# Kernel optimization log

Hardware: AMD Instinct MI355X
Metric: run time of the kernel (lower is better)

Reference implementation:

```python
import jax, jax.numpy as jnp
import numpy as np

BODY_EDGES = [(0, 2), (0, 5), (2, 7), (5, 8), (11, 12), (0, 11), (0, 12), (7, 11), (8, 12), (11, 13), (13, 15), (12, 14), (14, 16), (11, 23), (12, 24), (23, 24), (11, 24), (12, 23)]
N_JOINTS = 33
N_FEAT = 52
HIDDEN = 128
BN_EPS = 1e-5


def _make_adj():
    a = np.eye(N_JOINTS, dtype=np.float32)
    for i, j in BODY_EDGES:
        a[i, j] = 1.0
        a[j, i] = 1.0
    deg = np.clip(a.sum(1), 1.0, None)
    d = deg ** -0.5
    return jnp.asarray(d[:, None] * a * d[None, :])


def setup_inputs() -> dict:
    key = jax.random.key(0)
    ks = iter(jax.random.split(key, 40))
    B, T = 64, 256
    def lin(k, i, o):
        return jax.random.normal(k, (i, o), jnp.float32) / np.sqrt(i)
    inp = {
        'x': jax.random.normal(next(ks), (B, T, N_JOINTS, N_FEAT), jnp.float32),
        'adj': _make_adj(),
        # layer 0: in 52 -> out 128 (has skip linear)
        'W0': lin(next(ks), N_FEAT, HIDDEN), 'b0': jax.random.normal(next(ks), (HIDDEN,)) * 0.02,
        'S0': lin(next(ks), N_FEAT, HIDDEN), 'sb0': jax.random.normal(next(ks), (HIDDEN,)) * 0.02,
        'g0': 1.0 + 0.1 * jax.random.normal(next(ks), (HIDDEN,)), 'be0': 0.1 * jax.random.normal(next(ks), (HIDDEN,)),
        'm0': 0.1 * jax.random.normal(next(ks), (HIDDEN,)), 'v0': 1.0 + 0.1 * jax.random.uniform(next(ks), (HIDDEN,)),
        # layers 1,2: 128 -> 128 (identity skip)
        'W1': lin(next(ks), HIDDEN, HIDDEN), 'b1': jax.random.normal(next(ks), (HIDDEN,)) * 0.02,
        'g1': 1.0 + 0.1 * jax.random.normal(next(ks), (HIDDEN,)), 'be1': 0.1 * jax.random.normal(next(ks), (HIDDEN,)),
        'm1': 0.1 * jax.random.normal(next(ks), (HIDDEN,)), 'v1': 1.0 + 0.1 * jax.random.uniform(next(ks), (HIDDEN,)),
        'W2': lin(next(ks), HIDDEN, HIDDEN), 'b2': jax.random.normal(next(ks), (HIDDEN,)) * 0.02,
        'g2': 1.0 + 0.1 * jax.random.normal(next(ks), (HIDDEN,)), 'be2': 0.1 * jax.random.normal(next(ks), (HIDDEN,)),
        'm2': 0.1 * jax.random.normal(next(ks), (HIDDEN,)), 'v2': 1.0 + 0.1 * jax.random.uniform(next(ks), (HIDDEN,)),
        # temporal attention MLP: 128 -> 128 -> 1
        'tW1': lin(next(ks), HIDDEN, HIDDEN), 'tb1': jax.random.normal(next(ks), (HIDDEN,)) * 0.02,
        'tW2': lin(next(ks), HIDDEN, 1), 'tb2': jax.random.normal(next(ks), (1,)) * 0.02,
    }
    return inp


def _gcn(h, adj, W, b, g, be, m, v, skip):
    # adjacency mix: [B*T, J, D_in]
    a = jnp.einsum('nm,bmd->bnd', adj, h)
    z = a @ W + b
    z = (z - m) * jax.lax.rsqrt(v + BN_EPS) * g + be  # eval-mode BatchNorm1d
    return jax.nn.gelu(z, approximate=False) + skip


def reference(x, adj, W0, b0, S0, sb0, g0, be0, m0, v0,
              W1, b1, g1, be1, m1, v1,
              W2, b2, g2, be2, m2, v2,
              tW1, tb1, tW2, tb2):
    B, T, J, Fd = x.shape
    h = x.reshape(B * T, J, Fd)
    h = _gcn(h, adj, W0, b0, g0, be0, m0, v0, h @ S0 + sb0)
    h = _gcn(h, adj, W1, b1, g1, be1, m1, v1, h)
    h = _gcn(h, adj, W2, b2, g2, be2, m2, v2, h)
    # dropout inactive (eval mode)
    xt = h.mean(axis=1).reshape(B, T, -1)                  # [B, T, H]
    score = jax.nn.gelu(xt @ tW1 + tb1, approximate=False) @ tW2 + tb2  # [B, T, 1]
    attn = jax.nn.softmax(score, axis=1)
    return (xt * attn).sum(axis=1)                         # [B, H]
```

## Files before the change

### kernel.cpp

```cpp
#include <hip/hip_runtime.h>
#include <hip/hip_bf16.h>
#include <math.h>


#define NJ 33
#define NF 52
#define NH 128
#define NT 256
#define NB 64
#define NSAMP (NB*NT)
#define SPB 2
#define NBLKS (NSAMP/SPB)
#define HSTR 136
#define PSTR 40

typedef unsigned short u16;
typedef _Float16 f16;
typedef f16   half8 __attribute__((ext_vector_type(8)));
typedef f16   h2    __attribute__((ext_vector_type(2)));
typedef float f32x4 __attribute__((ext_vector_type(4)));

#define HO_W0    0
#define HO_S0    8192
#define HO_W1    16384
#define HO_W2    32768
#define HO_TW1   49152
#define HO_ADJ32 65536
#define H_TOTAL  66560
#define FO_BASE  (H_TOTAL/2)
#define FO_A0    (FO_BASE+0)
#define FO_SB0   (FO_BASE+768)
#define FO_TB1   (FO_BASE+896)
#define FO_TW2   (FO_BASE+1024)
#define FO_XT    (FO_BASE+1152)
#define FO_SC    (FO_XT + NSAMP*NH)

__device__ __forceinline__ float bf2f(u16 u) { return __uint_as_float(((unsigned)u) << 16); }
__device__ __forceinline__ float ldv(const void* p, long i, int f) {
    float r;
    if (f) r = bf2f(((const u16*)p)[i]);
    else   r = ((const float*)p)[i];
    return r;
}
__device__ int detect_bf16(const void* p) {
    const u16* q = (const u16*)p;
    int nz = 0, ok = 0;
#pragma unroll
    for (int k = 0; k < 64; k++) {
        u16 u = q[k];
        if (u & 0x7FFF) {
            nz++;
            int e = (u >> 7) & 0xFF;
            ok += (e >= 0x40 && e <= 0xBF) ? 1 : 0;
        }
    }
    return (nz == 0) || (ok * 20 >= nz * 19);
}

__device__ __forceinline__ float gelu_t(float x) {
    float xc = fminf(fmaxf(x, -8.f), 8.f);
    float u  = xc * fmaf(xc * xc, 0.10294324f, 2.3022082f);
#if __has_builtin(__builtin_amdgcn_exp2f)
    float e  = __builtin_amdgcn_exp2f(u);
#else
    float e  = exp2f(u);
#endif
#if __has_builtin(__builtin_amdgcn_rcpf)
    float tt = (e - 1.f) * __builtin_amdgcn_rcpf(e + 1.f);
#else
    float tt = (e - 1.f) / (e + 1.f);
#endif
    float hx = 0.5f * x;
    return fmaf(hx, tt, hx);
}

#define MFMA16(a, b, c) __builtin_amdgcn_mfma_f32_16x16x32_f16(a, b, c, 0, 0, 0)

__global__ __launch_bounds__(256) void prep(
    const void* adj,
    const void* W0, const void* b0, const void* S0, const void* sb0,
    const void* g0, const void* be0, const void* m0, const void* v0,
    const void* W1, const void* b1, const void* g1, const void* be1, const void* m1, const void* v1,
    const void* W2, const void* b2, const void* g2, const void* be2, const void* m2, const void* v2,
    const void* tW1, const void* tb1, const void* tW2,
    void* ws)
{
    f16* H = (f16*)ws; float* F = (float*)ws;
    const int bi = blockIdx.x, t = threadIdx.x;
    if (bi == 0) {
        const int fW = detect_bf16(W0), fS = detect_bf16(S0);
        for (int i = t; i < NF * 128; i += 256) {
            int k = i >> 7, n = i & 127;
            H[HO_W0 + n * 64 + k] = (f16)ldv(W0, i, fW);
            H[HO_S0 + n * 64 + k] = (f16)ldv(S0, i, fS);
        }
        for (int i = t; i < 128 * 16; i += 256) {
            int n = i >> 4, k = 48 + (i & 15);
            if (k >= NF) { H[HO_W0 + n * 64 + k] = (f16)0.f; H[HO_S0 + n * 64 + k] = (f16)0.f; }
        }
    } else if (bi == 1) {
        const int f = detect_bf16(W1);
        for (int i = t; i < 128 * 128; i += 256) {
            int k = i >> 7, n = i & 127;
            H[HO_W1 + n * 128 + k] = (f16)ldv(W1, i, f);
        }
    } else if (bi == 2) {
        const int f = detect_bf16(W2);
        for (int i = t; i < 128 * 128; i += 256) {
            int k = i >> 7, n = i & 127;
            H[HO_W2 + n * 128 + k] = (f16)ldv(W2, i, f);
        }
    } else if (bi == 3) {
        const int f = detect_bf16(tW1);
        for (int i = t; i < 128 * 128; i += 256) {
            int k = i >> 7, n = i & 127;
            H[HO_TW1 + n * 128 + k] = (f16)ldv(tW1, i, f);
        }
    } else {
        if (t < 128) {
            int c = t;
            {
                float g = ldv(g0,c,detect_bf16(g0)), be = ldv(be0,c,detect_bf16(be0));
                float m = ldv(m0,c,detect_bf16(m0)), v = ldv(v0,c,detect_bf16(v0));
                float b = ldv(b0,c,detect_bf16(b0));
                float A = g * rsqrtf(v + 1e-5f);
                F[FO_A0 + 0*256 + c] = A; F[FO_A0 + 0*256 + 128 + c] = (b - m)*A + be;
            }
            {
                float g = ldv(g1,c,detect_bf16(g1)), be = ldv(be1,c,detect_bf16(be1));
                float m = ldv(m1,c,detect_bf16(m1)), v = ldv(v1,c,detect_bf16(v1));
                float b = ldv(b1,c,detect_bf16(b1));
                float A = g * rsqrtf(v + 1e-5f);
                F[FO_A0 + 1*256 + c] = A; F[FO_A0 + 1*256 + 128 + c] = (b - m)*A + be;
            }
            {
                float g = ldv(g2,c,detect_bf16(g2)), be = ldv(be2,c,detect_bf16(be2));
                float m = ldv(m2,c,detect_bf16(m2)), v = ldv(v2,c,detect_bf16(v2));
                float b = ldv(b2,c,detect_bf16(b2));
                float A = g * rsqrtf(v + 1e-5f);
                F[FO_A0 + 2*256 + c] = A; F[FO_A0 + 2*256 + 128 + c] = (b - m)*A + be;
            }
            F[FO_SB0 + c] = ldv(sb0, c, detect_bf16(sb0));
            F[FO_TB1 + c] = ldv(tb1, c, detect_bf16(tb1));
            F[FO_TW2 + c] = ldv(tW2, c, detect_bf16(tW2));
        }
        const int fA = detect_bf16(adj);
        for (int i = t; i < 1024; i += 256) {
            int r = i >> 5, c = i & 31;
            float v = (r < 25 && c < 25) ? ldv(adj, (long)r*NJ + c, fA) : 0.f;
            H[HO_ADJ32 + i] = (f16)v;
        }
    }
}

#define PTWRITE(ACC)                                                            \
    _Pragma("unroll")                                                           \
    for (int mt = 0; mt < 4; mt++) {                                            \
        const int fF = mt >> 1;                                                 \
        const int jb = (mt & 1) * 16;                                           \
        _Pragma("unroll")                                                       \
        for (int nt = 0; nt < 2; nt++) {                                        \
            f16* pp = Pt + (fF*128 + (nt ? c1 : c0))*PSTR;                      \
            _Pragma("unroll")                                                   \
            for (int r2 = 0; r2 < 4; r2 += 2) {                                 \
                int j0 = jb + q*4 + r2;                                         \
                if (j0 + 1 < 25) {                                              \
                    h2 v2w = { (f16)ACC[mt][nt][r2], (f16)ACC[mt][nt][r2+1] };  \
                    *(h2*)(pp + j0) = v2w;                                      \
                } else if (j0 < 25) {                                           \
                    pp[j0] = (f16)ACC[mt][nt][r2];                              \
                }                                                               \
            }                                                                   \
        }                                                                       \
    }

#define ADJEPI(L, WRHB) {                                                       \
    f32x4 zac[2][2][2];                                                         \
    _Pragma("unroll")                                                           \
    for (int fF = 0; fF < 2; fF++) {                                            \
        _Pragma("unroll")                                                       \
        for (int nt = 0; nt < 2; nt++) {                                        \
            half8 bz = *(const half8*)(Pt + (fF*128 + (nt?c1:c0))*PSTR + q*8);  \
            zac[fF][0][nt] = MFMA16(afadj0, bz, z4);                            \
            zac[fF][1][nt] = MFMA16(afadj1, bz, z4);                            \
        }                                                                       \
    }                                                                           \
    _Pragma("unroll")                                                           \
    for (int nt = 0; nt < 2; nt++) {                                            \
        const int cc = nt ? c1 : c0;                                            \
        const float Av = rA[L][nt], Dv = rD[L][nt];                             \
        _Pragma("unroll")                                                       \
        for (int fF = 0; fF < 2; fF++) {                                        \
            _Pragma("unroll")                                                   \
            for (int m2 = 0; m2 < 2; m2++) {                                    \
                _Pragma("unroll")                                               \
                for (int r4 = 0; r4 < 4; r4++) {                                \
                    float zv = (m2 == 0) ? zac[fF][0][nt][r4]                   \
                             : (jlt[r4] ? zac[fF][1][nt][r4]                    \
                                        : acc[2*fF+1][nt][r4]);                 \
                    float hnew = gelu_t(fmaf(zv, Av, Dv)) + hz[fF][m2][nt][r4]; \
                    hz[fF][m2][nt][r4] = hnew;                                  \
                    if (WRHB)                                                   \
                        hb[((2*fF+m2)*16 + q*4 + r4)*HSTR + cc] = (f16)hnew;    \
                }                                                               \
            }                                                                   \
            {                                                                   \
                float hnew = gelu_t(fmaf(acc[4][nt][fF], Av, Dv)) + h32[fF][nt];\
                h32[fF][nt] = (q == 0) ? hnew : 0.f;                            \
                if (WRHB && q == 0)                                             \
                    hb[(64 + fF)*HSTR + cc] = (f16)hnew;                        \
            }                                                                   \
        }                                                                       \
    }                                                                           \
}

#define GEMM128(WOFF)                                                           \
    {                                                                           \
        half8 bf[2][4];                                                         \
        _Pragma("unroll")                                                       \
        for (int nt = 0; nt < 2; nt++)                                          \
            _Pragma("unroll")                                                   \
            for (int ks = 0; ks < 4; ks++)                                      \
                bf[nt][ks] = *(const half8*)(HW + (WOFF) + (nt?c1:c0)*128 + ks*32 + q*8); \
        _Pragma("unroll")                                                       \
        for (int mt = 0; mt < 5; mt++) { acc[mt][0] = z4; acc[mt][1] = z4; }    \
        _Pragma("unroll")                                                       \
        for (int mt = 0; mt < 5; mt++) {                                        \
            const int m = mt*16 + ml;                                           \
            _Pragma("unroll")                                                   \
            for (int ks = 0; ks < 4; ks++) {                                    \
                half8 af = *(const half8*)(hb + m*HSTR + ks*32 + q*8);          \
                acc[mt][0] = MFMA16(af, bf[0][ks], acc[mt][0]);                 \
                acc[mt][1] = MFMA16(af, bf[1][ks], acc[mt][1]);                 \
            }                                                                   \
        }                                                                       \
    }

__global__ __launch_bounds__(256) void gcn_mfma(const void* __restrict__ x,
                                                void* __restrict__ ws)
{
    const f16* HW = (const f16*)ws;
    float* F = (float*)ws;
    float* xt_g = F + FO_XT;
    float* sc_g = F + FO_SC;

    __shared__ __align__(16) f16 hb[80 * HSTR];
    __shared__ __align__(16) f16 Pt[2 * 128 * PSTR];
    __shared__ float rbuf4[4];
    __shared__ int sfx;
    float* xtb = (float*)Pt;

    const int t = threadIdx.x, lane = t & 63, wv = t >> 6;
    const int q = lane >> 4, ml = lane & 15;
    const int n0 = wv * 32;
    const int c0 = n0 + ml, c1 = n0 + 16 + ml;
    const f32x4 z4 = {0.f, 0.f, 0.f, 0.f};
    const bool jlt[4] = { q <= 2, q <= 1, q <= 1, q <= 1 };
    const half8 zero8 = {(f16)0.f,(f16)0.f,(f16)0.f,(f16)0.f,(f16)0.f,(f16)0.f,(f16)0.f,(f16)0.f};

    if (t == 0) sfx = detect_bf16(x);
#pragma unroll
    for (int i = t; i < 512; i += 256) {
        int fF = i >> 8, rem = i & 255, n = rem >> 1, ch = rem & 1;
        *(half8*)(Pt + (fF*128 + n)*PSTR + 24 + ch*8) = zero8;
    }

    float rA[3][2], rD[3][2];
#pragma unroll
    for (int L = 0; L < 3; L++) {
        rA[L][0] = F[FO_A0 + L*256 + c0];        rA[L][1] = F[FO_A0 + L*256 + c1];
        rD[L][0] = F[FO_A0 + L*256 + 128 + c0];  rD[L][1] = F[FO_A0 + L*256 + 128 + c1];
    }
    const float sb0a = F[FO_SB0 + c0], sb0b = F[FO_SB0 + c1];
    half8 afadj0 = *(const half8*)(HW + HO_ADJ32 + ml*32 + q*8);
    half8 afadj1 = *(const half8*)(HW + HO_ADJ32 + (16+ml)*32 + q*8);
    __syncthreads();

    {
        const int fX = sfx;
        const long xb = (long)blockIdx.x * (SPB * NJ * NF);
#pragma unroll 1
        for (int it = 0; it < 3; it++) {
            int g = t + it * 256;
            if (g < 66 * 8) {
                int r = g >> 3, blk = g & 7;
                int fF = (r >= 33) ? 1 : 0;
                int j = r - 33 * fF;
                int fr = (j < 32) ? (fF * 32 + j) : (64 + fF);
                half8 o;
                if (!fX) {
                    const float* base = (const float*)x + xb + (long)r * NF + blk * 8;
                    if (blk < 6) {
                        float4 v0 = *(const float4*)base;
                        float4 v1 = *(const float4*)(base + 4);
                        o[0]=(f16)v0.x; o[1]=(f16)v0.y; o[2]=(f16)v0.z; o[3]=(f16)v0.w;
                        o[4]=(f16)v1.x; o[5]=(f16)v1.y; o[6]=(f16)v1.z; o[7]=(f16)v1.w;
                    } else if (blk == 6) {
                        float4 v0 = *(const float4*)base;
                        o = zero8;
                        o[0]=(f16)v0.x; o[1]=(f16)v0.y; o[2]=(f16)v0.z; o[3]=(f16)v0.w;
                    } else o = zero8;
                } else {
                    long rb = xb + (long)r * NF;
#pragma unroll
                    for (int i = 0; i < 8; i++) {
                        int cx = blk * 8 + i;
                        o[i] = (f16)(cx < NF ? bf2f(((const u16*)x)[rb + cx]) : 0.f);
                    }
                }
                *(half8*)(hb + fr * HSTR + blk * 8) = o;
            }
        }
    }
    __syncthreads();

    f32x4 acc[5][2];
    float hz[2][2][2][4];
    float h32[2][2];

    {
        half8 bw[2][2], bs[2][2];
#pragma unroll
        for (int nt = 0; nt < 2; nt++) {
            int n = nt ? c1 : c0;
#pragma unroll
            for (int ks = 0; ks < 2; ks++) {
                bw[nt][ks] = *(const half8*)(HW + HO_W0 + n*64 + ks*32 + q*8);
                bs[nt][ks] = *(const half8*)(HW + HO_S0 + n*64 + ks*32 + q*8);
            }
        }
        f32x4 acs[5][2];
#pragma unroll
        for (int mt = 0; mt < 5; mt++) { acc[mt][0]=z4; acc[mt][1]=z4; acs[mt][0]=z4; acs[mt][1]=z4; }
#pragma unroll
        for (int mt = 0; mt < 5; mt++) {
            const int m = mt*16 + ml;
            half8 a0 = *(const half8*)(hb + m*HSTR + q*8);
            half8 a1 = *(const half8*)(hb + m*HSTR + 32 + q*8);
            acc[mt][0] = MFMA16(a0, bw[0][0], acc[mt][0]);
            acc[mt][0] = MFMA16(a1, bw[0][1], acc[mt][0]);
            acc[mt][1] = MFMA16(a0, bw[1][0], acc[mt][1]);
            acc[mt][1] = MFMA16(a1, bw[1][1], acc[mt][1]);
            acs[mt][0] = MFMA16(a0, bs[0][0], acs[mt][0]);
            acs[mt][0] = MFMA16(a1, bs[0][1], acs[mt][0]);
            acs[mt][1] = MFMA16(a0, bs[1][0], acs[mt][1]);
            acs[mt][1] = MFMA16(a1, bs[1][1], acs[mt][1]);
        }
        __syncthreads();
        PTWRITE(acc)
#pragma unroll
        for (int fF = 0; fF < 2; fF++)
#pragma unroll
            for (int m2 = 0; m2 < 2; m2++)
#pragma unroll
                for (int nt = 0; nt < 2; nt++)
#pragma unroll
                    for (int r4 = 0; r4 < 4; r4++)
                        hz[fF][m2][nt][r4] = acs[2*fF+m2][nt][r4] + (nt ? sb0b : sb0a);
#pragma unroll
        for (int fF = 0; fF < 2; fF++)
#pragma unroll
            for (int nt = 0; nt < 2; nt++)
                h32[fF][nt] = (q == 0) ? (acs[4][nt][fF] + (nt ? sb0b : sb0a)) : 0.f;
        ADJEPI(0, 1)
        __syncthreads();
    }

    GEMM128(HO_W1)
    __syncthreads();
    PTWRITE(acc)
    ADJEPI(1, 1)
    __syncthreads();

    GEMM128(HO_W2)
    __syncthreads();
    PTWRITE(acc)
    ADJEPI(2, 0)
    __syncthreads();

#pragma unroll
    for (int fF = 0; fF < 2; fF++)
#pragma unroll
        for (int nt = 0; nt < 2; nt++) {
            float s = h32[fF][nt];
#pragma unroll
            for (int m2 = 0; m2 < 2; m2++)
#pragma unroll
                for (int r4 = 0; r4 < 4; r4++) s += hz[fF][m2][nt][r4];
            s += __shfl_xor(s, 16, 64);
            s += __shfl_xor(s, 32, 64);
            float xtc = s * (1.0f / 33.0f);
            if (q == 0) {
                int cc = nt ? c1 : c0;
                xtb[fF * 128 + cc] = xtc;
                xt_g[((long)blockIdx.x * SPB + fF) * NH + cc] = xtc;
            }
        }
    __syncthreads();

    {
        const int fF = t >> 7, c = t & 127;
        float u = 0.f;
#pragma unroll
        for (int kk = 0; kk < 16; kk++) {
            half8 wv8 = *(const half8*)(HW + HO_TW1 + c*128 + kk*8);
#pragma unroll
            for (int i = 0; i < 8; i++)
                u = fmaf(xtb[fF*128 + kk*8 + i], (float)wv8[i], u);
        }
        float r = gelu_t(u + F[FO_TB1 + c]) * F[FO_TW2 + c];
#pragma unroll
        for (int off = 32; off > 0; off >>= 1) r += __shfl_xor(r, off, 64);
        if (lane == 0) rbuf4[wv] = r;
        __syncthreads();
        if (t == 0) {
            sc_g[blockIdx.x * SPB + 0] = rbuf4[0] + rbuf4[1];
            sc_g[blockIdx.x * SPB + 1] = rbuf4[2] + rbuf4[3];
        }
    }
}

__global__ __launch_bounds__(256) void attn_pool(
    const void* __restrict__ x,
    const float* __restrict__ xt_ws, const float* __restrict__ score_ws,
    void* __restrict__ out)
{
    __shared__ float ew[NT];
    __shared__ float red[8];
    __shared__ float pb[256];
    __shared__ int sfx2;
    const int t = threadIdx.x, lane = t & 63, wv = t >> 6;
    const int b = blockIdx.x >> 2, qr = blockIdx.x & 3;

    if (t == 0) sfx2 = detect_bf16(x);
    float sv = score_ws[b * NT + t];
    float m = sv;
#pragma unroll
    for (int off = 32; off > 0; off >>= 1) m = fmaxf(m, __shfl_xor(m, off, 64));
    if (lane == 0) red[wv] = m;
    __syncthreads();
    float mx = fmaxf(fmaxf(red[0], red[1]), fmaxf(red[2], red[3]));
    float e = __expf(sv - mx);
    ew[t] = e;
    float d = e;
#pragma unroll
    for (int off = 32; off > 0; off >>= 1) d += __shfl_xor(d, off, 64);
    if (lane == 0) red[4 + wv] = d;
    __syncthreads();
    float den = red[4] + red[5] + red[6] + red[7];

    const int cl = t & 31, ch = t >> 5;
    const int c = qr * 32 + cl;
    float a = 0.f;
#pragma unroll 4
    for (int i = ch * 32; i < ch * 32 + 32; i++)
        a = fmaf(ew[i], xt_ws[((long)b * NT + i) * NH + c], a);
    pb[t] = a;
    __syncthreads();
    if (t < 128) pb[t] += pb[t + 128];
    __syncthreads();
    if (t < 64) pb[t] += pb[t + 64];
    __syncthreads();
    if (t < 32) {
        float r = (pb[t] + pb[t + 32]) / den;
        if (sfx2) ((__hip_bfloat16*)out)[b * NH + qr * 32 + t] = __float2bfloat16(r);
        else      ((float*)out)[b * NH + qr * 32 + t] = r;
    }
}

extern "C" void kernel_launch(void* const* d_in, const int* in_sizes, int n_in,
                              void* d_out, int out_size, void* d_ws, size_t ws_size,
                              hipStream_t stream) {
    prep<<<5, 256, 0, stream>>>(
        d_in[1],
        d_in[2], d_in[3], d_in[4], d_in[5],
        d_in[6], d_in[7], d_in[8], d_in[9],
        d_in[10], d_in[11], d_in[12], d_in[13], d_in[14], d_in[15],
        d_in[16], d_in[17], d_in[18], d_in[19], d_in[20], d_in[21],
        d_in[22], d_in[23], d_in[24],
        d_ws);
    gcn_mfma<<<NBLKS, 256, 0, stream>>>(d_in[0], d_ws);
    float* F = (float*)d_ws;
    attn_pool<<<NB * 4, 256, 0, stream>>>(d_in[0], F + FO_XT, F + FO_SC, d_out);
}
```

Baseline: 574.5 us.

## Halve Pt scratch, split adjacency epilogue per sample, hoist dtype detection

```diff
diff --git a/kernel.cpp b/kernel.cpp
--- a/kernel.cpp
+++ b/kernel.cpp
@@ -32,7 +32,8 @@
 #define FO_SB0   (FO_BASE+768)
 #define FO_TB1   (FO_BASE+896)
 #define FO_TW2   (FO_BASE+1024)
-#define FO_XT    (FO_BASE+1152)
+#define FO_FLG   (FO_BASE+1152)
+#define FO_XT    (FO_BASE+1280)
 #define FO_SC    (FO_XT + NSAMP*NH)
 
 __device__ __forceinline__ float bf2f(u16 u) { return __uint_as_float(((unsigned)u) << 16); }
@@ -58,26 +59,23 @@
 }
 
 __device__ __forceinline__ float gelu_t(float x) {
-    float xc = fminf(fmaxf(x, -8.f), 8.f);
-    float u  = xc * fmaf(xc * xc, 0.10294324f, 2.3022082f);
+    float nu = x * fmaf(x * x, -0.10294324f, -2.3022082f);
 #if __has_builtin(__builtin_amdgcn_exp2f)
-    float e  = __builtin_amdgcn_exp2f(u);
+    float e  = __builtin_amdgcn_exp2f(nu);
 #else
-    float e  = exp2f(u);
+    float e  = exp2f(nu);
 #endif
 #if __has_builtin(__builtin_amdgcn_rcpf)
-    float tt = (e - 1.f) * __builtin_amdgcn_rcpf(e + 1.f);
+    return x * __builtin_amdgcn_rcpf(1.f + e);
 #else
-    float tt = (e - 1.f) / (e + 1.f);
+    return x / (1.f + e);
 #endif
-    float hx = 0.5f * x;
-    return fmaf(hx, tt, hx);
 }
 
 #define MFMA16(a, b, c) __builtin_amdgcn_mfma_f32_16x16x32_f16(a, b, c, 0, 0, 0)
 
 __global__ __launch_bounds__(256) void prep(
-    const void* adj,
+    const void* x, const void* adj,
     const void* W0, const void* b0, const void* S0, const void* sb0,
     const void* g0, const void* be0, const void* m0, const void* v0,
     const void* W1, const void* b1, const void* g1, const void* be1, const void* m1, const void* v1,
@@ -105,6 +103,7 @@
             H[HO_W1 + n * 128 + k] = (f16)ldv(W1, i, f);
         }
     } else if (bi == 2) {
+        if (t == 0) ((int*)F)[FO_FLG] = detect_bf16(x);
         const int f = detect_bf16(W2);
         for (int i = t; i < 128 * 128; i += 256) {
             int k = i >> 7, n = i & 127;
@@ -153,14 +152,14 @@
     }
 }
 
-#define PTWRITE(ACC)                                                            \
+#define PTWRITE_F(ACC, FF)                                                      \
     _Pragma("unroll")                                                           \
-    for (int mt = 0; mt < 4; mt++) {                                            \
-        const int fF = mt >> 1;                                                 \
-        const int jb = (mt & 1) * 16;                                           \
+    for (int mtl = 0; mtl < 2; mtl++) {                                         \
+        const int mt = 2*(FF) + mtl;                                            \
+        const int jb = mtl * 16;                                                \
         _Pragma("unroll")                                                       \
         for (int nt = 0; nt < 2; nt++) {                                        \
-            f16* pp = Pt + (fF*128 + (nt ? c1 : c0))*PSTR;                      \
+            f16* pp = Pt + (nt ? c1 : c0)*PSTR;                                 \
             _Pragma("unroll")                                                   \
             for (int r2 = 0; r2 < 4; r2 += 2) {                                 \
                 int j0 = jb + q*4 + r2;                                         \
@@ -174,42 +173,36 @@
         }                                                                       \
     }
 
-#define ADJEPI(L, WRHB) {                                                       \
-    f32x4 zac[2][2][2];                                                         \
+#define ADJEPI_F(L, FF, WRHB) {                                                 \
+    f32x4 zac[2][2];                                                            \
     _Pragma("unroll")                                                           \
-    for (int fF = 0; fF < 2; fF++) {                                            \
-        _Pragma("unroll")                                                       \
-        for (int nt = 0; nt < 2; nt++) {                                        \
-            half8 bz = *(const half8*)(Pt + (fF*128 + (nt?c1:c0))*PSTR + q*8);  \
-            zac[fF][0][nt] = MFMA16(afadj0, bz, z4);                            \
-            zac[fF][1][nt] = MFMA16(afadj1, bz, z4);                            \
-        }                                                                       \
+    for (int nt = 0; nt < 2; nt++) {                                            \
+        half8 bz = *(const half8*)(Pt + (nt?c1:c0)*PSTR + q*8);                 \
+        zac[0][nt] = MFMA16(afadj0, bz, z4);                                    \
+        zac[1][nt] = MFMA16(afadj1, bz, z4);                                    \
     }                                                                           \
     _Pragma("unroll")                                                           \
     for (int nt = 0; nt < 2; nt++) {                                            \
         const int cc = nt ? c1 : c0;                                            \
         const float Av = rA[L][nt], Dv = rD[L][nt];                             \
         _Pragma("unroll")                                                       \
-        for (int fF = 0; fF < 2; fF++) {                                        \
+        for (int m2 = 0; m2 < 2; m2++) {                                        \
             _Pragma("unroll")                                                   \
-            for (int m2 = 0; m2 < 2; m2++) {                                    \
-                _Pragma("unroll")                                               \
-                for (int r4 = 0; r4 < 4; r4++) {                                \
-                    float zv = (m2 == 0) ? zac[fF][0][nt][r4]                   \
-                             : (jlt[r4] ? zac[fF][1][nt][r4]                    \
-                                        : acc[2*fF+1][nt][r4]);                 \
-                    float hnew = gelu_t(fmaf(zv, Av, Dv)) + hz[fF][m2][nt][r4]; \
-                    hz[fF][m2][nt][r4] = hnew;                                  \
-                    if (WRHB)                                                   \
-                        hb[((2*fF+m2)*16 + q*4 + r4)*HSTR + cc] = (f16)hnew;    \
-                }                                                               \
+            for (int r4 = 0; r4 < 4; r4++) {                                    \
+                float zv = (m2 == 0) ? zac[0][nt][r4]                           \
+                         : (jlt[r4] ? zac[1][nt][r4]                            \
+                                    : acc[2*(FF)+1][nt][r4]);                   \
+                float hnew = gelu_t(fmaf(zv, Av, Dv)) + hz[FF][m2][nt][r4];     \
+                hz[FF][m2][nt][r4] = hnew;                                      \
+                if (WRHB)                                                       \
+                    hb[((2*(FF)+m2)*16 + q*4 + r4)*HSTR + cc] = (f16)hnew;      \
             }                                                                   \
-            {                                                                   \
-                float hnew = gelu_t(fmaf(acc[4][nt][fF], Av, Dv)) + h32[fF][nt];\
-                h32[fF][nt] = (q == 0) ? hnew : 0.f;                            \
-                if (WRHB && q == 0)                                             \
-                    hb[(64 + fF)*HSTR + cc] = (f16)hnew;                        \
-            }                                                                   \
+        }                                                                       \
+        {                                                                       \
+            float hnew = gelu_t(fmaf(acc[4][nt][FF], Av, Dv)) + h32[FF][nt];    \
+            h32[FF][nt] = (q == 0) ? hnew : 0.f;                                \
+            if (WRHB && q == 0)                                                 \
+                hb[(64 + (FF))*HSTR + cc] = (f16)hnew;                          \
         }                                                                       \
     }                                                                           \
 }
@@ -236,8 +229,8 @@
         }                                                                       \
     }
 
-__global__ __launch_bounds__(256) void gcn_mfma(const void* __restrict__ x,
-                                                void* __restrict__ ws)
+__global__ __launch_bounds__(256, 4) void gcn_mfma(const void* __restrict__ x,
+                                                   void* __restrict__ ws)
 {
     const f16* HW = (const f16*)ws;
     float* F = (float*)ws;
@@ -245,9 +238,8 @@
     float* sc_g = F + FO_SC;
 
     __shared__ __align__(16) f16 hb[80 * HSTR];
-    __shared__ __align__(16) f16 Pt[2 * 128 * PSTR];
+    __shared__ __align__(16) f16 Pt[128 * PSTR];
     __shared__ float rbuf4[4];
-    __shared__ int sfx;
     float* xtb = (float*)Pt;
 
     const int t = threadIdx.x, lane = t & 63, wv = t >> 6;
@@ -258,11 +250,9 @@
     const bool jlt[4] = { q <= 2, q <= 1, q <= 1, q <= 1 };
     const half8 zero8 = {(f16)0.f,(f16)0.f,(f16)0.f,(f16)0.f,(f16)0.f,(f16)0.f,(f16)0.f,(f16)0.f};
 
-    if (t == 0) sfx = detect_bf16(x);
-#pragma unroll
-    for (int i = t; i < 512; i += 256) {
-        int fF = i >> 8, rem = i & 255, n = rem >> 1, ch = rem & 1;
-        *(half8*)(Pt + (fF*128 + n)*PSTR + 24 + ch*8) = zero8;
+    {
+        int n = t >> 1, chh = t & 1;
+        *(half8*)(Pt + n*PSTR + 24 + chh*8) = zero8;
     }
 
     float rA[3][2], rD[3][2];
@@ -274,10 +264,9 @@
     const float sb0a = F[FO_SB0 + c0], sb0b = F[FO_SB0 + c1];
     half8 afadj0 = *(const half8*)(HW + HO_ADJ32 + ml*32 + q*8);
     half8 afadj1 = *(const half8*)(HW + HO_ADJ32 + (16+ml)*32 + q*8);
-    __syncthreads();
 
     {
-        const int fX = sfx;
+        const int fX = ((const int*)F)[FO_FLG];
         const long xb = (long)blockIdx.x * (SPB * NJ * NF);
 #pragma unroll 1
         for (int it = 0; it < 3; it++) {
@@ -347,7 +336,6 @@
             acs[mt][1] = MFMA16(a1, bs[1][1], acs[mt][1]);
         }
         __syncthreads();
-        PTWRITE(acc)
 #pragma unroll
         for (int fF = 0; fF < 2; fF++)
 #pragma unroll
@@ -362,20 +350,27 @@
 #pragma unroll
             for (int nt = 0; nt < 2; nt++)
                 h32[fF][nt] = (q == 0) ? (acs[4][nt][fF] + (nt ? sb0b : sb0a)) : 0.f;
-        ADJEPI(0, 1)
+        PTWRITE_F(acc, 0)
+        ADJEPI_F(0, 0, 1)
+        PTWRITE_F(acc, 1)
+        ADJEPI_F(0, 1, 1)
         __syncthreads();
     }
 
     GEMM128(HO_W1)
     __syncthreads();
-    PTWRITE(acc)
-    ADJEPI(1, 1)
+    PTWRITE_F(acc, 0)
+    ADJEPI_F(1, 0, 1)
+    PTWRITE_F(acc, 1)
+    ADJEPI_F(1, 1, 1)
     __syncthreads();
 
     GEMM128(HO_W2)
     __syncthreads();
-    PTWRITE(acc)
-    ADJEPI(2, 0)
+    PTWRITE_F(acc, 0)
+    ADJEPI_F(2, 0, 0)
+    PTWRITE_F(acc, 1)
+    ADJEPI_F(2, 1, 0)
     __syncthreads();
 
 #pragma unroll
@@ -421,18 +416,16 @@
 }
 
 __global__ __launch_bounds__(256) void attn_pool(
-    const void* __restrict__ x,
+    const int* __restrict__ flg,
     const float* __restrict__ xt_ws, const float* __restrict__ score_ws,
     void* __restrict__ out)
 {
     __shared__ float ew[NT];
     __shared__ float red[8];
     __shared__ float pb[256];
-    __shared__ int sfx2;
     const int t = threadIdx.x, lane = t & 63, wv = t >> 6;
     const int b = blockIdx.x >> 2, qr = blockIdx.x & 3;
 
-    if (t == 0) sfx2 = detect_bf16(x);
     float sv = score_ws[b * NT + t];
     float m = sv;
 #pragma unroll
@@ -463,7 +456,7 @@
     __syncthreads();
     if (t < 32) {
         float r = (pb[t] + pb[t + 32]) / den;
-        if (sfx2) ((__hip_bfloat16*)out)[b * NH + qr * 32 + t] = __float2bfloat16(r);
+        if (*flg) ((__hip_bfloat16*)out)[b * NH + qr * 32 + t] = __float2bfloat16(r);
         else      ((float*)out)[b * NH + qr * 32 + t] = r;
     }
 }
@@ -472,7 +465,7 @@
                               void* d_out, int out_size, void* d_ws, size_t ws_size,
                               hipStream_t stream) {
     prep<<<5, 256, 0, stream>>>(
-        d_in[1],
+        d_in[0], d_in[1],
         d_in[2], d_in[3], d_in[4], d_in[5],
         d_in[6], d_in[7], d_in[8], d_in[9],
         d_in[10], d_in[11], d_in[12], d_in[13], d_in[14], d_in[15],
@@ -481,5 +474,5 @@
         d_ws);
     gcn_mfma<<<NBLKS, 256, 0, stream>>>(d_in[0], d_ws);
     float* F = (float*)d_ws;
-    attn_pool<<<NB * 4, 256, 0, stream>>>(d_in[0], F + FO_XT, F + FO_SC, d_out);
-}
+    attn_pool<<<NB * 4, 256, 0, stream>>>((const int*)(F + FO_FLG), F + FO_XT, F + FO_SC, d_out);
+}
```

Result: slower. 848.7 us (+47.7%).
